# Kernel optimization log

Measured on AMD Instinct MI355X. Metric: run time of the kernel, lower is better.

Reference implementation:

```python
import jax, jax.numpy as jnp
import numpy as np

N_TP = 4  # number of heterogeneous agent types (experts)


def _mlp(x, w1, b1, w2, b2, w3, b3):
    h = jax.nn.relu(x @ w1 + b1)
    h = jax.nn.relu(h @ w2 + b2)
    return h @ w3 + b3


def setup_inputs() -> dict:
    key = jax.random.key(0)
    ks = jax.random.split(key, 12)
    T, A, D, H, NA = 2048, 128, 64, 64, 16
    s = 0.05
    return {
        "obs": jax.random.normal(ks[0], (T, A, D), dtype=jnp.float32),
        "hete_pick": jax.random.randint(ks[1], (T, A), 0, N_TP, dtype=jnp.int64),
        "gp_sel_summary": jax.random.uniform(ks[2], (T, N_TP), dtype=jnp.float32),
        "W1": jax.random.normal(ks[3], (N_TP, D + N_TP, H), dtype=jnp.float32) * s,
        "b1": jnp.zeros((N_TP, H), jnp.float32),
        "W2": jax.random.normal(ks[4], (N_TP, H, H), dtype=jnp.float32) * s,
        "b2": jnp.zeros((N_TP, H), jnp.float32),
        "W3": jax.random.normal(ks[5], (N_TP, H, NA), dtype=jnp.float32) * s,
        "b3": jnp.zeros((N_TP, NA), jnp.float32),
        "cW1": jax.random.normal(ks[6], (D + N_TP, H), dtype=jnp.float32) * s,
        "cb1": jnp.zeros((H,), jnp.float32),
        "cW2": jax.random.normal(ks[7], (H, H), dtype=jnp.float32) * s,
        "cb2": jnp.zeros((H,), jnp.float32),
        "cW3": jax.random.normal(ks[8], (H, 1), dtype=jnp.float32) * s,
        "cb3": jnp.zeros((1,), jnp.float32),
    }


def reference(obs, hete_pick, gp_sel_summary, W1, b1, W2, b2, W3, b3,
              cW1, cb1, cW2, cb2, cW3, cb3):
    T, A, D = obs.shape
    n_tp = W1.shape[0]
    # hete_info_obs: broadcast group-selection summary over agents, concat to obs
    hete_info = jnp.broadcast_to(gp_sel_summary[:, None, :], (T, A, n_tp))
    x = jnp.concatenate([obs, hete_info.astype(obs.dtype)], axis=-1)  # [T,A,D+n_tp]
    xf = x.reshape(T * A, D + n_tp)
    tp = hete_pick.reshape(T * A)
    # per-type dispatch: mask -> sub-net -> scatter back (expressed as masked select)
    logits = jnp.zeros((T * A, W3.shape[-1]), obs.dtype)
    for t in range(n_tp):
        out_t = _mlp(xf, W1[t], b1[t], W2[t], b2[t], W3[t], b3[t])
        logits = jnp.where((tp == t)[:, None], out_t, logits)
    # central critic runs on all agents
    value = _mlp(xf, cW1, cb1, cW2, cb2, cW3, cb3)  # [T*A,1]
    out = jnp.concatenate([logits, value], axis=-1)  # [T*A, n_action+1]
    return out.reshape(T, A, -1)
```

## Files before the change

kernel.cpp:

```cpp
#include <hip/hip_runtime.h>
#include <stdint.h>


typedef float v4f __attribute__((ext_vector_type(4)));
typedef short v8s __attribute__((ext_vector_type(8)));

#define NTOK   262144
#define XS_STR 104
#define HS_STR 136
#define WP2_OFF 30720
#define WP3_OFF 51200

static __device__ __forceinline__ short f2bf(float f) {
    union { float f; uint32_t u; } c; c.f = f;
    uint32_t u = c.u;
    uint32_t r = (u + 0x7FFFu + ((u >> 16) & 1u)) >> 16;
    return (short)r;
}


__global__ void count_kernel(const int* __restrict__ hete, int* __restrict__ hdr) {
    __shared__ int wc[4][4];
    int tid = threadIdx.x, lane = tid & 63, w = tid >> 6;
    int i = blockIdx.x * 256 + tid;
    int e = hete[i];
#pragma unroll
    for (int t = 0; t < 4; t++) {
        unsigned long long m = __ballot(e == t);
        if (lane == 0) wc[w][t] = __popcll(m);
    }
    __syncthreads();
    if (tid < 4) {
        int s = wc[0][tid] + wc[1][tid] + wc[2][tid] + wc[3][tid];
        atomicAdd(&hdr[tid], s);
    }
}

__global__ void prefix_kernel(int* __restrict__ hdr, int* __restrict__ bucket) {
    __shared__ int sa[5], sc[4];
    int tid = threadIdx.x;
    if (tid == 0) {
        int a = 0, ts = 0;
        for (int e = 0; e < 4; e++) {
            int c = hdr[e];
            sc[e] = c;
            sa[e] = a;
            hdr[4 + e]  = a;
            hdr[8 + e]  = a;
            hdr[13 + e] = ts;
            int tiles = (c + 127) >> 7;
            a  += tiles << 7;
            ts += tiles;
        }
        sa[4]   = a;
        hdr[12] = a;
        hdr[17] = ts;
    }
    __syncthreads();
    for (int e = 0; e < 4; e++) {
        int start = sa[e] + sc[e];
        int end   = sa[e + 1];
        for (int i = start + tid; i < end; i += 256) bucket[i] = -1;
    }
}

__global__ void scatter_kernel(const int* __restrict__ hete, int* __restrict__ hdr,
                               int* __restrict__ bucket) {
    __shared__ int wc[4][4], wb[4][4];
    int tid = threadIdx.x, lane = tid & 63, w = tid >> 6;
    int i = blockIdx.x * 256 + tid;
    int e = hete[i];
    unsigned long long lt = (1ull << lane) - 1ull;
    int rank = 0;
#pragma unroll
    for (int t = 0; t < 4; t++) {
        unsigned long long m = __ballot(e == t);
        if (lane == 0) wc[w][t] = __popcll(m);
        if (e == t) rank = __popcll(m & lt);
    }
    __syncthreads();
    if (tid < 4) {
        int t = tid, tot = 0;
#pragma unroll
        for (int ww = 0; ww < 4; ww++) tot += wc[ww][t];
        int base = atomicAdd(&hdr[4 + t], tot);
#pragma unroll
        for (int ww = 0; ww < 4; ww++) { int c = wc[ww][t]; wb[ww][t] = base; base += c; }
    }
    __syncthreads();
    bucket[wb[w][e] + rank] = i;
}


__global__ void prep_kernel(const float* __restrict__ W1, const float* __restrict__ cW1,
                            const float* __restrict__ W2, const float* __restrict__ cW2,
                            const float* __restrict__ W3, const float* __restrict__ cW3,
                            short* __restrict__ wp) {
    int b = blockIdx.x, lane = threadIdx.x;
    int nl = lane & 15, quad = lane >> 4;
    short frag[8];
    if (b < 60) {
        int e = b / 12, rem = b % 12, ks = rem / 4, nt = rem % 4;
        int n = nt * 16 + nl;
#pragma unroll
        for (int j = 0; j < 8; j++) {
            int k = ks * 32 + quad * 8 + j;
            float v = 0.f;
            if (k < 68) v = (e < 4) ? W1[(e * 68 + k) * 64 + n] : cW1[k * 64 + n];
            frag[j] = f2bf(v);
        }
    } else if (b < 100) {
        int u = b - 60, e = u / 8, ks = (u % 8) / 4, nt = u % 4;
        int n = nt * 16 + nl;
#pragma unroll
        for (int j = 0; j < 8; j++) {
            int k = ks * 32 + quad * 8 + j;
            frag[j] = f2bf((e < 4) ? W2[(e * 64 + k) * 64 + n] : cW2[k * 64 + n]);
        }
    } else {
        int u = b - 100;
#pragma unroll
        for (int j = 0; j < 8; j++) {
            int ks = (u < 8) ? (u & 1) : (u - 8);
            int k  = ks * 32 + quad * 8 + j;
            float v;
            if (u < 8) { int ee = u >> 1; v = W3[(ee * 64 + k) * 16 + nl]; }
            else       { v = (nl == 0) ? cW3[k] : 0.f; }
            frag[j] = f2bf(v);
        }
    }
    v8s pk = { frag[0], frag[1], frag[2], frag[3], frag[4], frag[5], frag[6], frag[7] };
    *(v8s*)(wp + (size_t)b * 512 + lane * 8) = pk;
}


__global__ __launch_bounds__(256) void main_kernel(
    const float* __restrict__ obs, const float* __restrict__ gp,
    const int* __restrict__ bucket, const int* __restrict__ hdr,
    const short* __restrict__ wp,
    const float* __restrict__ b1, const float* __restrict__ b2, const float* __restrict__ b3,
    const float* __restrict__ cb1, const float* __restrict__ cb2, const float* __restrict__ cb3,
    float* __restrict__ out)
{
    __shared__ __align__(16) short xs[128 * XS_STR];
    __shared__ __align__(16) short hs[128 * HS_STR];
    __shared__ int tokL[128];

    int b = blockIdx.x;
    int total = hdr[17];
    if (b >= total) return;
    int e = 3;
    if      (b < hdr[14]) e = 0;
    else if (b < hdr[15]) e = 1;
    else if (b < hdr[16]) e = 2;
    int slot0 = hdr[8 + e] + (b - hdr[13 + e]) * 128;

    int tid = threadIdx.x, lane = tid & 63, w = tid >> 6;
    int ml = lane & 15, quad = lane >> 4;

    if (tid < 128) tokL[tid] = bucket[slot0 + tid];

    {
        int r = tid >> 1, hh = tid & 1;
        int tk = bucket[slot0 + r];
        v8s z = { 0, 0, 0, 0, 0, 0, 0, 0 };
        if (tk >= 0) {
            const float4* src = (const float4*)(obs + (size_t)tk * 64 + hh * 32);
#pragma unroll
            for (int t = 0; t < 4; t++) {
                float4 f0 = src[2 * t], f1 = src[2 * t + 1];
                v8s pk = { f2bf(f0.x), f2bf(f0.y), f2bf(f0.z), f2bf(f0.w),
                           f2bf(f1.x), f2bf(f1.y), f2bf(f1.z), f2bf(f1.w) };
                *(v8s*)&xs[r * XS_STR + hh * 32 + t * 8] = pk;
            }
            if (hh) {
                const float* g = gp + (size_t)(tk >> 7) * 4;
                v8s pg = { f2bf(g[0]), f2bf(g[1]), f2bf(g[2]), f2bf(g[3]), 0, 0, 0, 0 };
                *(v8s*)&xs[r * XS_STR + 64] = pg;
                *(v8s*)&xs[r * XS_STR + 72] = z;
                *(v8s*)&xs[r * XS_STR + 80] = z;
                *(v8s*)&xs[r * XS_STR + 88] = z;
            }
        } else {
#pragma unroll
            for (int t = 0; t < 4; t++) *(v8s*)&xs[r * XS_STR + hh * 32 + t * 8] = z;
            if (hh) {
                *(v8s*)&xs[r * XS_STR + 64] = z;
                *(v8s*)&xs[r * XS_STR + 72] = z;
                *(v8s*)&xs[r * XS_STR + 80] = z;
                *(v8s*)&xs[r * XS_STR + 88] = z;
            }
        }
    }
    __syncthreads();

    v4f accE[8], accC[8];
#pragma unroll
    for (int m = 0; m < 8; m++) { accE[m] = (v4f){0,0,0,0}; accC[m] = (v4f){0,0,0,0}; }
#pragma unroll
    for (int ks = 0; ks < 3; ks++) {
        v8s bE = *(const v8s*)(wp + (size_t)((e * 3 + ks) * 4 + w) * 512 + lane * 8);
        v8s bC = *(const v8s*)(wp + (size_t)((12 + ks) * 4 + w) * 512 + lane * 8);
#pragma unroll
        for (int m = 0; m < 8; m++) {
            v8s a = *(const v8s*)&xs[(m * 16 + ml) * XS_STR + ks * 32 + quad * 8];
            accE[m] = __builtin_amdgcn_mfma_f32_16x16x32_bf16(a, bE, accE[m], 0, 0, 0);
            accC[m] = __builtin_amdgcn_mfma_f32_16x16x32_bf16(a, bC, accC[m], 0, 0, 0);
        }
    }
    {
        float bE1 = b1[e * 64 + w * 16 + ml], bC1 = cb1[w * 16 + ml];
#pragma unroll
        for (int m = 0; m < 8; m++)
#pragma unroll
            for (int rr = 0; rr < 4; rr++) {
                int row = m * 16 + quad * 4 + rr;
                hs[row * HS_STR + w * 16 + ml]      = f2bf(fmaxf(accE[m][rr] + bE1, 0.f));
                hs[row * HS_STR + 64 + w * 16 + ml] = f2bf(fmaxf(accC[m][rr] + bC1, 0.f));
            }
    }
    __syncthreads();

    v4f acc2E[8], acc2C[8];
#pragma unroll
    for (int m = 0; m < 8; m++) { acc2E[m] = (v4f){0,0,0,0}; acc2C[m] = (v4f){0,0,0,0}; }
#pragma unroll
    for (int ks = 0; ks < 2; ks++) {
        v8s bE = *(const v8s*)(wp + WP2_OFF + (size_t)((e * 2 + ks) * 4 + w) * 512 + lane * 8);
        v8s bC = *(const v8s*)(wp + WP2_OFF + (size_t)((8 + ks) * 4 + w) * 512 + lane * 8);
#pragma unroll
        for (int m = 0; m < 8; m++) {
            v8s aE = *(const v8s*)&hs[(m * 16 + ml) * HS_STR + ks * 32 + quad * 8];
            v8s aC = *(const v8s*)&hs[(m * 16 + ml) * HS_STR + 64 + ks * 32 + quad * 8];
            acc2E[m] = __builtin_amdgcn_mfma_f32_16x16x32_bf16(aE, bE, acc2E[m], 0, 0, 0);
            acc2C[m] = __builtin_amdgcn_mfma_f32_16x16x32_bf16(aC, bC, acc2C[m], 0, 0, 0);
        }
    }
    __syncthreads();
    {
        float bE2 = b2[e * 64 + w * 16 + ml], bC2 = cb2[w * 16 + ml];
#pragma unroll
        for (int m = 0; m < 8; m++)
#pragma unroll
            for (int rr = 0; rr < 4; rr++) {
                int row = m * 16 + quad * 4 + rr;
                hs[row * HS_STR + w * 16 + ml]      = f2bf(fmaxf(acc2E[m][rr] + bE2, 0.f));
                hs[row * HS_STR + 64 + w * 16 + ml] = f2bf(fmaxf(acc2C[m][rr] + bC2, 0.f));
            }
    }
    __syncthreads();

    v4f accL[2], accV[2];
#pragma unroll
    for (int mm = 0; mm < 2; mm++) { accL[mm] = (v4f){0,0,0,0}; accV[mm] = (v4f){0,0,0,0}; }
#pragma unroll
    for (int ks = 0; ks < 2; ks++) {
        v8s bW = *(const v8s*)(wp + WP3_OFF + (size_t)(e * 2 + ks) * 512 + lane * 8);
        v8s bV = *(const v8s*)(wp + WP3_OFF + (size_t)(8 + ks) * 512 + lane * 8);
#pragma unroll
        for (int mm = 0; mm < 2; mm++) {
            v8s aE = *(const v8s*)&hs[((2 * w + mm) * 16 + ml) * HS_STR + ks * 32 + quad * 8];
            v8s aC = *(const v8s*)&hs[((2 * w + mm) * 16 + ml) * HS_STR + 64 + ks * 32 + quad * 8];
            accL[mm] = __builtin_amdgcn_mfma_f32_16x16x32_bf16(aE, bW, accL[mm], 0, 0, 0);
            accV[mm] = __builtin_amdgcn_mfma_f32_16x16x32_bf16(aC, bV, accV[mm], 0, 0, 0);
        }
    }

    {
        float b3v = b3[e * 16 + ml], cb3v = cb3[0];
#pragma unroll
        for (int mm = 0; mm < 2; mm++)
#pragma unroll
            for (int rr = 0; rr < 4; rr++) {
                int row = (2 * w + mm) * 16 + quad * 4 + rr;
                int tk = tokL[row];
                if (tk >= 0) {
                    float* o = out + (size_t)tk * 17;
                    o[ml] = accL[mm][rr] + b3v;
                    if (ml == 0) o[16] = accV[mm][rr] + cb3v;
                }
            }
    }
}


extern "C" void kernel_launch(void* const* d_in, const int* in_sizes, int n_in,
                              void* d_out, int out_size, void* d_ws, size_t ws_size,
                              hipStream_t stream) {
    const float* obs = (const float*)d_in[0];
    const int*  hete = (const int*)d_in[1];
    const float* gp  = (const float*)d_in[2];
    const float* W1  = (const float*)d_in[3];
    const float* b1  = (const float*)d_in[4];
    const float* W2  = (const float*)d_in[5];
    const float* b2  = (const float*)d_in[6];
    const float* W3  = (const float*)d_in[7];
    const float* b3  = (const float*)d_in[8];
    const float* cW1 = (const float*)d_in[9];
    const float* cb1 = (const float*)d_in[10];
    const float* cW2 = (const float*)d_in[11];
    const float* cb2 = (const float*)d_in[12];
    const float* cW3 = (const float*)d_in[13];
    const float* cb3 = (const float*)d_in[14];
    float* out = (float*)d_out;

    int*   hdr    = (int*)d_ws;
    int*   bucket = hdr + 32;
    short* wp     = (short*)(bucket + 262656);

    hipMemsetAsync(hdr, 0, 128, stream);
    count_kernel  <<<1024, 256, 0, stream>>>(hete, hdr);
    prefix_kernel <<<1,    256, 0, stream>>>(hdr, bucket);
    scatter_kernel<<<1024, 256, 0, stream>>>(hete, hdr, bucket);
    prep_kernel   <<<110,   64, 0, stream>>>(W1, cW1, W2, cW2, W3, cW3, wp);
    main_kernel   <<<2051, 256, 0, stream>>>(obs, gp, bucket, hdr, wp,
                                             b1, b2, b3, cb1, cb2, cb3, out);
}
```

Baseline: 194.4 us.

## Replace global atomic bucketing with per-block counts and prefix scan; alias LDS buffers

Token bucketing by expert now has each of 256 blocks count 1024 tokens into its own slot. A single-block scan then computes per-block base offsets, and scatter uses shared-memory atomics on those offsets. This removes the memset and the global atomic contention on the header counters. Separately, main_kernel aliases the xs and hs shared buffers into one array, with an extra barrier before the overwrite, to cut LDS use and raise occupancy. Bucket order within an expert becomes block-ordered but is still nondeterministic within a block.

After: 159.7 us. -17.8%, faster.

```diff
diff --git a/kernel.cpp b/kernel.cpp
--- a/kernel.cpp
+++ b/kernel.cpp
@@ -5,7 +5,6 @@
 typedef float v4f __attribute__((ext_vector_type(4)));
 typedef short v8s __attribute__((ext_vector_type(8)));
 
-#define NTOK   262144
 #define XS_STR 104
 #define HS_STR 136
 #define WP2_OFF 30720
@@ -19,33 +18,52 @@
 }
 
 
-__global__ void count_kernel(const int* __restrict__ hete, int* __restrict__ hdr) {
+__global__ void count_kernel(const int* __restrict__ hete, int* __restrict__ cnt) {
     __shared__ int wc[4][4];
     int tid = threadIdx.x, lane = tid & 63, w = tid >> 6;
-    int i = blockIdx.x * 256 + tid;
-    int e = hete[i];
-#pragma unroll
-    for (int t = 0; t < 4; t++) {
-        unsigned long long m = __ballot(e == t);
-        if (lane == 0) wc[w][t] = __popcll(m);
-    }
-    __syncthreads();
-    if (tid < 4) {
-        int s = wc[0][tid] + wc[1][tid] + wc[2][tid] + wc[3][tid];
-        atomicAdd(&hdr[tid], s);
-    }
-}
-
-__global__ void prefix_kernel(int* __restrict__ hdr, int* __restrict__ bucket) {
-    __shared__ int sa[5], sc[4];
+    int base = blockIdx.x * 1024;
+    int lc[4] = {0, 0, 0, 0};
+#pragma unroll
+    for (int c = 0; c < 4; c++) {
+        int e = hete[base + c * 256 + tid];
+#pragma unroll
+        for (int t = 0; t < 4; t++) {
+            unsigned long long m = __ballot(e == t);
+            if (lane == 0) lc[t] += __popcll(m);
+        }
+    }
+    if (lane == 0)
+#pragma unroll
+        for (int t = 0; t < 4; t++) wc[w][t] = lc[t];
+    __syncthreads();
+    if (tid < 4)
+        cnt[blockIdx.x * 4 + tid] = wc[0][tid] + wc[1][tid] + wc[2][tid] + wc[3][tid];
+}
+
+__global__ void prefix_kernel(const int* __restrict__ cnt, int* __restrict__ hdr,
+                              int* __restrict__ bb, int* __restrict__ bucket) {
+    __shared__ int s[4][256];
+    __shared__ int sa[5], sC[4];
     int tid = threadIdx.x;
+    int c0[4];
+#pragma unroll
+    for (int t = 0; t < 4; t++) { c0[t] = cnt[tid * 4 + t]; s[t][tid] = c0[t]; }
+    __syncthreads();
+    for (int off = 1; off < 256; off <<= 1) {
+        int v[4];
+#pragma unroll
+        for (int t = 0; t < 4; t++) v[t] = (tid >= off) ? s[t][tid - off] : 0;
+        __syncthreads();
+#pragma unroll
+        for (int t = 0; t < 4; t++) s[t][tid] += v[t];
+        __syncthreads();
+    }
     if (tid == 0) {
         int a = 0, ts = 0;
         for (int e = 0; e < 4; e++) {
-            int c = hdr[e];
-            sc[e] = c;
+            int c = s[e][255];
+            sC[e] = c;
             sa[e] = a;
-            hdr[4 + e]  = a;
             hdr[8 + e]  = a;
             hdr[13 + e] = ts;
             int tiles = (c + 127) >> 7;
@@ -57,40 +75,38 @@
         hdr[17] = ts;
     }
     __syncthreads();
+#pragma unroll
+    for (int t = 0; t < 4; t++) bb[tid * 4 + t] = sa[t] + s[t][tid] - c0[t];
     for (int e = 0; e < 4; e++) {
-        int start = sa[e] + sc[e];
-        int end   = sa[e + 1];
+        int start = sa[e] + sC[e], end = sa[e + 1];
         for (int i = start + tid; i < end; i += 256) bucket[i] = -1;
     }
 }
 
-__global__ void scatter_kernel(const int* __restrict__ hete, int* __restrict__ hdr,
+__global__ void scatter_kernel(const int* __restrict__ hete, const int* __restrict__ bb,
                                int* __restrict__ bucket) {
-    __shared__ int wc[4][4], wb[4][4];
-    int tid = threadIdx.x, lane = tid & 63, w = tid >> 6;
-    int i = blockIdx.x * 256 + tid;
-    int e = hete[i];
+    __shared__ int cur[4];
+    int tid = threadIdx.x, lane = tid & 63;
+    if (tid < 4) cur[tid] = bb[blockIdx.x * 4 + tid];
+    __syncthreads();
     unsigned long long lt = (1ull << lane) - 1ull;
-    int rank = 0;
-#pragma unroll
-    for (int t = 0; t < 4; t++) {
-        unsigned long long m = __ballot(e == t);
-        if (lane == 0) wc[w][t] = __popcll(m);
-        if (e == t) rank = __popcll(m & lt);
-    }
-    __syncthreads();
-    if (tid < 4) {
-        int t = tid, tot = 0;
-#pragma unroll
-        for (int ww = 0; ww < 4; ww++) tot += wc[ww][t];
-        int base = atomicAdd(&hdr[4 + t], tot);
-#pragma unroll
-        for (int ww = 0; ww < 4; ww++) { int c = wc[ww][t]; wb[ww][t] = base; base += c; }
-    }
-    __syncthreads();
-    bucket[wb[w][e] + rank] = i;
-}
-
+#pragma unroll
+    for (int c = 0; c < 4; c++) {
+        int i = blockIdx.x * 1024 + c * 256 + tid;
+        int e = hete[i];
+        int slot = 0;
+#pragma unroll
+        for (int t = 0; t < 4; t++) {
+            unsigned long long m = __ballot(e == t);
+            int n = __popcll(m);
+            int wb = 0;
+            if (lane == 0 && n) wb = atomicAdd(&cur[t], n);
+            wb = __shfl(wb, 0);
+            if (e == t) slot = wb + __popcll(m & lt);
+        }
+        bucket[slot] = i;
+    }
+}
 
 __global__ void prep_kernel(const float* __restrict__ W1, const float* __restrict__ cW1,
                             const float* __restrict__ W2, const float* __restrict__ cW2,
@@ -142,9 +158,10 @@
     const float* __restrict__ cb1, const float* __restrict__ cb2, const float* __restrict__ cb3,
     float* __restrict__ out)
 {
-    __shared__ __align__(16) short xs[128 * XS_STR];
-    __shared__ __align__(16) short hs[128 * HS_STR];
+    __shared__ __align__(16) short buf[128 * HS_STR];
     __shared__ int tokL[128];
+    short* xs = buf;
+    short* hs = buf;
 
     int b = blockIdx.x;
     int total = hdr[17];
@@ -208,6 +225,7 @@
             accC[m] = __builtin_amdgcn_mfma_f32_16x16x32_bf16(a, bC, accC[m], 0, 0, 0);
         }
     }
+    __syncthreads();
     {
         float bE1 = b1[e * 64 + w * 16 + ml], bC1 = cb1[w * 16 + ml];
 #pragma unroll
@@ -306,13 +324,14 @@
 
     int*   hdr    = (int*)d_ws;
     int*   bucket = hdr + 32;
-    short* wp     = (short*)(bucket + 262656);
-
-    hipMemsetAsync(hdr, 0, 128, stream);
-    count_kernel  <<<1024, 256, 0, stream>>>(hete, hdr);
-    prefix_kernel <<<1,    256, 0, stream>>>(hdr, bucket);
-    scatter_kernel<<<1024, 256, 0, stream>>>(hete, hdr, bucket);
-    prep_kernel   <<<110,   64, 0, stream>>>(W1, cW1, W2, cW2, W3, cW3, wp);
+    int*   cnt    = bucket + 262656;
+    int*   bb     = cnt + 1024;
+    short* wp     = (short*)(bb + 1024);
+
+    count_kernel  <<<256, 256, 0, stream>>>(hete, cnt);
+    prefix_kernel <<<1,   256, 0, stream>>>(cnt, hdr, bb, bucket);
+    scatter_kernel<<<256, 256, 0, stream>>>(hete, bb, bucket);
+    prep_kernel   <<<110,  64, 0, stream>>>(W1, cW1, W2, cW2, W3, cW3, wp);
     main_kernel   <<<2051, 256, 0, stream>>>(obs, gp, bucket, hdr, wp,
                                              b1, b2, b3, cb1, cb2, cb3, out);
 }
```
